# Kernel optimization log

Hardware: AMD Instinct MI355X
Metric: run time of the kernel (lower is better)

## Reference

```python
import jax, jax.numpy as jnp
import numpy as np
import math

LENS = 64  # sliding window length (init arg `lens`)

def setup_inputs() -> dict:
    key = jax.random.key(0)
    k1, k2 = jax.random.split(key)
    N, D = 4096, 512
    X = jax.random.normal(k1, (N, D), dtype=jnp.float32)
    # nn.Linear(d, d, bias=False) weight, applied as x @ W.T
    W = jax.random.normal(k2, (D, D), dtype=jnp.float32) * (1.0 / math.sqrt(D))
    return {"X": X, "W": W}

def reference(X, W):
    N, d = X.shape
    B = N - LENS  # number of sliding windows
    # sliding-window gather: h_his[b] = X[b : b+LENS]
    idx = jnp.arange(B)[:, None] + jnp.arange(LENS)[None, :]  # [B, LENS]
    h_his = X[idx]            # [B, LENS, d]
    h_cur = X[LENS:]          # [B, d]  (index_cur = lens..N-1)
    # attention: score = bmm(linear(kv), q[..., None]) / sqrt(d)
    kv_proj = jnp.einsum('bld,ed->ble', h_his, W)            # [B, LENS, d]
    score = jnp.einsum('ble,be->bl', kv_proj, h_cur)[..., None] / math.sqrt(d)  # [B, LENS, 1]
    # faithful to original: softmax over last (size-1) axis -> all ones
    alpha = jax.nn.softmax(score, axis=-1)                   # [B, LENS, 1]
    attn_out = jnp.einsum('bl,bld->bd', alpha[..., 0], h_his)  # [B, d]
    # dropout(0.3) is eval-mode identity
    H = jnp.concatenate([X[:LENS], attn_out], axis=0) + X    # [N, d]
    h_cur_full = jnp.concatenate([X[:LENS], h_cur], axis=0)  # [N, d]
    return jnp.concatenate([H, h_cur_full], axis=-1)         # [N, 2d]
```

## Files before the change

kernel.cpp:

```cpp
#include <hip/hip_runtime.h>


#define LENS 64
#define RT 8
#define C4 128

__global__ __launch_bounds__(256) void winsum_kernel(const float4* __restrict__ X4,
                                                     float4* __restrict__ O4,
                                                     int N) {
    const int c4   = threadIdx.x & (C4 - 1);
    const int half = threadIdx.x >> 7;
    const int i0   = blockIdx.x * (2 * RT) + half * RT;
    if (i0 >= N) return;

    if (i0 < LENS) {
        for (int k = 0; k < RT; ++k) {
            const int i = i0 + k;
            float4 x = X4[(size_t)i * C4 + c4];
            float4 h = make_float4(2.f * x.x, 2.f * x.y, 2.f * x.z, 2.f * x.w);
            O4[(size_t)i * (2 * C4) + c4]      = h;
            O4[(size_t)i * (2 * C4) + C4 + c4] = x;
        }
        return;
    }

    float4 hist[RT - 1];
    float4 w = make_float4(0.f, 0.f, 0.f, 0.f);
    const float4* p = X4 + (size_t)(i0 - LENS) * C4 + c4;
#pragma unroll
    for (int j = 0; j < LENS; ++j) {
        float4 x = p[(size_t)j * C4];
        if (j < RT - 1) hist[j] = x;
        w.x += x.x; w.y += x.y; w.z += x.z; w.w += x.w;
    }

#pragma unroll
    for (int k = 0; k < RT; ++k) {
        const int i = i0 + k;
        float4 x = X4[(size_t)i * C4 + c4];
        float4 h = make_float4(x.x + w.x, x.y + w.y, x.z + w.z, x.w + w.w);
        O4[(size_t)i * (2 * C4) + c4]      = h;
        O4[(size_t)i * (2 * C4) + C4 + c4] = x;
        if (k < RT - 1) {
            float4 old = hist[k];
            w.x += x.x - old.x;
            w.y += x.y - old.y;
            w.z += x.z - old.z;
            w.w += x.w - old.w;
        }
    }
}

extern "C" void kernel_launch(void* const* d_in, const int* in_sizes, int n_in,
                              void* d_out, int out_size, void* d_ws, size_t ws_size,
                              hipStream_t stream) {
    const float* X = (const float*)d_in[0];
    float* O = (float*)d_out;

    const int D = 512;
    const int N = in_sizes[0] / D;

    const int rows_per_block = 2 * RT;
    const int grid = (N + rows_per_block - 1) / rows_per_block;
    winsum_kernel<<<grid, 256, 0, stream>>>((const float4*)X, (float4*)O, N);
}
```

Before: 80.68 us.

## Precompute 8-row chunk sums to shorten sliding-window initial sum

Adds a pre-pass kernel that sums every aligned group of 8 rows into a workspace buffer. The main kernel now builds its initial 64-row window sum from 8 chunk sums instead of reading 64 rows, and loads only the 7 history rows it needs. This cuts the per-thread load count and memory traffic in the main kernel, at the cost of a second launch and a workspace write/read. It relies on i0 being a multiple of 8 and on the workspace being large enough.

```diff
diff --git a/kernel.cpp b/kernel.cpp
--- a/kernel.cpp
+++ b/kernel.cpp
@@ -5,7 +5,25 @@
 #define RT 8
 #define C4 128
 
+__global__ __launch_bounds__(256) void chunk8_kernel(const float4* __restrict__ X4,
+                                                     float4* __restrict__ C8,
+                                                     int nChunks) {
+    const int t  = blockIdx.x * 256 + threadIdx.x;
+    const int c4 = t & (C4 - 1);
+    const int k  = t >> 7;
+    if (k >= nChunks) return;
+    const float4* p = X4 + (size_t)k * 8 * C4 + c4;
+    float4 s = make_float4(0.f, 0.f, 0.f, 0.f);
+#pragma unroll
+    for (int j = 0; j < 8; ++j) {
+        float4 x = p[(size_t)j * C4];
+        s.x += x.x; s.y += x.y; s.z += x.z; s.w += x.w;
+    }
+    C8[(size_t)k * C4 + c4] = s;
+}
+
 __global__ __launch_bounds__(256) void winsum_kernel(const float4* __restrict__ X4,
+                                                     const float4* __restrict__ C8,
                                                      float4* __restrict__ O4,
                                                      int N) {
     const int c4   = threadIdx.x & (C4 - 1);
@@ -14,6 +32,7 @@
     if (i0 >= N) return;
 
     if (i0 < LENS) {
+#pragma unroll
         for (int k = 0; k < RT; ++k) {
             const int i = i0 + k;
             float4 x = X4[(size_t)i * C4 + c4];
@@ -24,15 +43,18 @@
         return;
     }
 
+    const int m = i0 >> 3;
+    float4 w = make_float4(0.f, 0.f, 0.f, 0.f);
+#pragma unroll
+    for (int q = 0; q < 8; ++q) {
+        float4 cs = C8[(size_t)(m - 8 + q) * C4 + c4];
+        w.x += cs.x; w.y += cs.y; w.z += cs.z; w.w += cs.w;
+    }
+
     float4 hist[RT - 1];
-    float4 w = make_float4(0.f, 0.f, 0.f, 0.f);
-    const float4* p = X4 + (size_t)(i0 - LENS) * C4 + c4;
+    const float4* ph = X4 + (size_t)(i0 - LENS) * C4 + c4;
 #pragma unroll
-    for (int j = 0; j < LENS; ++j) {
-        float4 x = p[(size_t)j * C4];
-        if (j < RT - 1) hist[j] = x;
-        w.x += x.x; w.y += x.y; w.z += x.z; w.w += x.w;
-    }
+    for (int j = 0; j < RT - 1; ++j) hist[j] = ph[(size_t)j * C4];
 
 #pragma unroll
     for (int k = 0; k < RT; ++k) {
@@ -56,11 +78,16 @@
                               hipStream_t stream) {
     const float* X = (const float*)d_in[0];
     float* O = (float*)d_out;
+    float* C = (float*)d_ws;
 
     const int D = 512;
     const int N = in_sizes[0] / D;
+    const int nChunks = N / 8;
+
+    chunk8_kernel<<<(nChunks * C4 + 255) / 256, 256, 0, stream>>>(
+        (const float4*)X, (float4*)C, nChunks);
 
     const int rows_per_block = 2 * RT;
-    const int grid = (N + rows_per_block - 1) / rows_per_block;
-    winsum_kernel<<<grid, 256, 0, stream>>>((const float4*)X, (float4*)O, N);
+    winsum_kernel<<<(N + rows_per_block - 1) / rows_per_block, 256, 0, stream>>>(
+        (const float4*)X, (const float4*)C, (float4*)O, N);
 }
```

Result: faster. 69.30 us (-14.1%).
